# Optimization experiments

Hardware: AMD Instinct MI355X
Metric: run time of the kernel (lower is better)

Reference implementation:

```python
import jax, jax.numpy as jnp
import numpy as np

B, C_IN, C_OUT, STYLE_DIM, H, W = 8, 512, 512, 512, 32, 32

def setup_inputs() -> dict:
    key = jax.random.key(0)
    k = jax.random.split(key, 7)
    x = jax.random.normal(k[0], (B, C_IN, H, W), dtype=jnp.float32)
    style = jax.random.normal(k[1], (B, STYLE_DIM), dtype=jnp.float32)
    noise = jax.random.normal(k[2], (B, 1, 2 * H, 2 * W), dtype=jnp.float32)
    # learned params (Conv2d weight, style_fc Linear, output bias)
    conv_w = jax.random.normal(k[3], (C_OUT, C_IN, 3, 3), dtype=jnp.float32) * 0.05
    fc_w = jax.random.normal(k[4], (C_IN, STYLE_DIM), dtype=jnp.float32) * 0.05
    fc_b = jax.random.normal(k[5], (C_IN,), dtype=jnp.float32) * 0.05
    bias = jnp.zeros((1, C_OUT, 1, 1), dtype=jnp.float32)
    return {"x": x, "style": style, "noise": noise,
            "conv_w": conv_w, "fc_w": fc_w, "fc_b": fc_b, "bias": bias}

def reference(x, style, noise, conv_w, fc_w, fc_b, bias):
    b, c, h, w = x.shape
    o = conv_w.shape[0]
    x = jnp.repeat(jnp.repeat(x, 2, axis=2), 2, axis=3)  # (B, C, 2H, 2W)
    # style modulation: (B, C)
    s = style @ fc_w.T + fc_b
    # per-sample modulated weight (B, O, C, 3, 3)
    wmod = conv_w[None] * (s[:, None, :, None, None] + 1.0)
    # demodulation
    d = jax.lax.rsqrt(jnp.sum(wmod * wmod, axis=(2, 3, 4)) + 1e-8)  # (B, O)
    wmod = wmod * d[:, :, None, None, None]
    # grouped conv: one group per batch sample
    xr = x.reshape(1, b * c, 2 * h, 2 * w)
    wr = wmod.reshape(b * o, c, 3, 3)
    y = jax.lax.conv_general_dilated(
        xr, wr, window_strides=(1, 1), padding='SAME',
        feature_group_count=b,
        dimension_numbers=('NCHW', 'OIHW', 'NCHW'))
    y = y.reshape(b, o, 2 * h, 2 * w) + bias + noise
    return jax.nn.leaky_relu(y, negative_slope=0.2)
```

## Files before the change

kernel.cpp:

```cpp
#include <hip/hip_runtime.h>

typedef short v8s __attribute__((ext_vector_type(8)));
typedef float f32x4 __attribute__((ext_vector_type(4)));
typedef unsigned short ushort_t;

#define BB    8
#define CIN   512
#define COUT  512
#define SDIM  512

#define GLDS(g, l)                                                      \
    __builtin_amdgcn_global_load_lds(                                   \
        (const __attribute__((address_space(1))) void*)(g),             \
        (__attribute__((address_space(3))) void*)(l), 16, 0, 0)

static __device__ __forceinline__ ushort_t f2bf(float f) {
    union { float f; unsigned u; } un; un.f = f;
    unsigned r = un.u + 0x7FFF + ((un.u >> 16) & 1);
    return (ushort_t)(r >> 16);
}

__global__ void k_prep1(const float* __restrict__ style, const float* __restrict__ fc_w,
                        const float* __restrict__ fc_b, float* __restrict__ m,
                        const float* __restrict__ conv_w, float* __restrict__ q,
                        ushort_t* __restrict__ Wb, float* __restrict__ guard) {
    __shared__ float sst[SDIM];
    const int bid = blockIdx.x;
    if (bid < 1024) {
        const int idx = bid * 256 + threadIdx.x;
        const int o = idx >> 9, c = idx & 511;
        float w[3][3];
        const float* wp = conv_w + idx * 9;
        float qs = 0.f;
        for (int i = 0; i < 3; i++)
            for (int j = 0; j < 3; j++) {
                float v = wp[i * 3 + j];
                w[i][j] = v;
                qs += v * v;
            }
        q[idx] = qs;
        const int ch = c >> 5, kg = (c >> 3) & 3, c8 = c & 7;
        for (int py = 0; py < 2; py++) {
            float rs[2][3];
            for (int kx = 0; kx < 3; kx++) {
                rs[0][kx] = (py == 0) ? w[0][kx] : w[0][kx] + w[1][kx];
                rs[1][kx] = (py == 0) ? w[1][kx] + w[2][kx] : w[2][kx];
            }
            for (int px = 0; px < 2; px++) {
                const int p = py * 2 + px;
                float vals[4];
                if (px == 0) {
                    vals[0] = rs[0][0];
                    vals[1] = rs[0][1] + rs[0][2];
                    vals[2] = rs[1][0];
                    vals[3] = rs[1][1] + rs[1][2];
                } else {
                    vals[0] = rs[0][0] + rs[0][1];
                    vals[1] = rs[0][2];
                    vals[2] = rs[1][0] + rs[1][1];
                    vals[3] = rs[1][2];
                }
                for (int t = 0; t < 4; t++)
                    Wb[(size_t)p * (16 * 4 * 4 * 512 * 8) + (size_t)ch * (4 * 4 * 512 * 8)
                       + ((size_t)(t * 4 + kg) * 512 + o) * 8 + c8] = f2bf(vals[t]);
            }
        }
    } else {
        const int sb = bid - 1024;
        const int bx = sb & 1, b = sb >> 1;
        if (sb == 0 && threadIdx.x < 8) guard[threadIdx.x] = 0.f;
        for (int k = threadIdx.x; k < SDIM; k += 256) sst[k] = style[b * SDIM + k];
        __syncthreads();
        const int c = bx * 256 + threadIdx.x;
        float acc = fc_b[c];
        const float* wr = fc_w + c * SDIM;
        for (int k = 0; k < SDIM; k += 4) {
            float4 w4 = *(const float4*)(wr + k);
            acc += w4.x * sst[k] + w4.y * sst[k + 1] + w4.z * sst[k + 2] + w4.w * sst[k + 3];
        }
        m[b * CIN + c] = acc + 1.0f;
    }
}

__global__ void k_prep2(const float* __restrict__ x, const float* __restrict__ m,
                        ushort_t* __restrict__ Xt, const float* __restrict__ q,
                        float* __restrict__ d) {
    __shared__ __align__(16) ushort_t lt[32 * 528];
    const int bid = blockIdx.x, t = threadIdx.x;
    if (bid < 256) {
        const int r = bid & 31, b = bid >> 5;
        for (int s = t; s < 4096; s += 256) {
            const int c = s >> 3, q4 = (s & 7) * 4;
            float4 v = *(const float4*)(x + (((size_t)(b * CIN + c) * 32 + r) * 32 + q4));
            const float mv = m[b * CIN + c];
            lt[(q4 + 0) * 528 + c] = f2bf(v.x * mv);
            lt[(q4 + 1) * 528 + c] = f2bf(v.y * mv);
            lt[(q4 + 2) * 528 + c] = f2bf(v.z * mv);
            lt[(q4 + 3) * 528 + c] = f2bf(v.w * mv);
        }
        __syncthreads();
        for (int s = t; s < 2048; s += 256) {
            const int qq = s >> 6, c8 = s & 63;
            v8s v = *(v8s*)&lt[qq * 528 + c8 * 8];
            *(v8s*)(Xt + (((size_t)(b * 32 + r) * 32 + qq) * 512 + c8 * 8)) = v;
        }
    } else {
        const int w = (bid - 256) * 4 + (t >> 6);
        const int L = t & 63;
        const int b = w >> 9, o = w & 511;
        float4 q1 = *(const float4*)(q + o * 512 + L * 8);
        float4 q2 = *(const float4*)(q + o * 512 + L * 8 + 4);
        float4 m1 = *(const float4*)(m + b * 512 + L * 8);
        float4 m2 = *(const float4*)(m + b * 512 + L * 8 + 4);
        float acc = m1.x * m1.x * q1.x + m1.y * m1.y * q1.y + m1.z * m1.z * q1.z +
                    m1.w * m1.w * q1.w + m2.x * m2.x * q2.x + m2.y * m2.y * q2.y +
                    m2.z * m2.z * q2.z + m2.w * m2.w * q2.w;
        for (int off = 32; off; off >>= 1) acc += __shfl_down(acc, off, 64);
        if (L == 0) d[w] = rsqrtf(acc + 1e-8f);
    }
}

__global__ __launch_bounds__(512, 2) void k_gemm(
    const ushort_t* __restrict__ Xt, const ushort_t* __restrict__ Wb,
    const float* __restrict__ dmod, const float* __restrict__ bias,
    const float* __restrict__ noise, float* __restrict__ out,
    const float* __restrict__ guard) {
    __shared__ __align__(16) ushort_t Wt[4][256 * 32];
    __shared__ __align__(16) ushort_t Xs[4][256 * 32];

    const int tid = threadIdx.x;
    const int L = tid & 63;
    const int wid = tid >> 6;

    const int lin = blockIdx.x + 2 * blockIdx.y + 8 * blockIdx.z;
    const int log = (lin & 7) * 32 + (lin >> 3);
    const int o0 = (log & 1) * 256;
    const int n0 = ((log >> 1) & 3) * 256;
    const int zz = log >> 3;
    const int b = zz >> 2, p = zz & 3;

    const int py = p >> 1, px = p & 1;
    const int ry0 = py ? 0 : -1, cx0 = px ? 0 : -1;
    const int wo = (wid >> 2) * 128, wn = (wid & 3) * 64;
    const int l15 = L & 15, l4 = L >> 4;

    const ushort_t* XtB = Xt + (size_t)b * (32 * 32 * 512);
    const ushort_t* WbP = Wb + (size_t)p * (16 * 4 * 4 * 512 * 8);

    f32x4 acc[8][4];
#pragma unroll
    for (int i = 0; i < 8; i++)
#pragma unroll
        for (int j = 0; j < 4; j++) acc[i][j] = {0.f, 0.f, 0.f, 0.f};

    auto stage1 = [&](int c0, ushort_t* wbuf, ushort_t* xbuf, int i) {
        const int slot = i * 512 + tid;
        const int row = slot >> 2;
        const int tap = (slot & 3) ^ ((row >> 1) & 3);
        const int ldo = (i * 512 + (tid & 448)) * 8;
        const ushort_t* wsrc =
            WbP + (size_t)(c0 >> 5) * (4 * 4 * 512 * 8)
            + ((size_t)((tap * 4 + ((c0 >> 3) & 3)) * 512 + o0 + row)) * 8;
        GLDS(wsrc, wbuf + ldo);
        const int pix = n0 + row;
        const int gr = (pix >> 5) + ry0 + (tap >> 1);
        const int gq = (pix & 31) + cx0 + (tap & 1);
        const ushort_t* xsrc =
            ((unsigned)gr < 32u && (unsigned)gq < 32u)
                ? XtB + (size_t)((gr * 32 + gq) * 512 + c0)
                : (const ushort_t*)guard;
        GLDS(xsrc, xbuf + ldo);
    };

    auto lread = [&](const ushort_t* buf, int row) -> v8s {
        const int gsel = l4 ^ ((row >> 1) & 3);
        return *(const v8s*)&buf[row * 32 + gsel * 8];
    };

#pragma unroll
    for (int pt = 0; pt < 3; ++pt) {
        stage1(pt * 8, Wt[pt], Xs[pt], 0);
        stage1(pt * 8, Wt[pt], Xs[pt], 1);
    }
    asm volatile("s_waitcnt vmcnt(8)" ::: "memory");
    __builtin_amdgcn_s_barrier();

    v8s bfr[4];
    for (int t = 0; t < 64; ++t) {
        const ushort_t* wb = Wt[t & 3];
        const ushort_t* xb = Xs[t & 3];
        ushort_t* wnb = Wt[(t + 3) & 3];
        ushort_t* xnb = Xs[(t + 3) & 3];
        const int c0n = (t + 3) * 8;
        const bool st = (t + 3) < 64;

        {
            v8s af[4];
#pragma unroll
            for (int i = 0; i < 4; i++) af[i] = lread(wb, wo + i * 16 + l15);
#pragma unroll
            for (int j = 0; j < 4; j++) bfr[j] = lread(xb, wn + j * 16 + l15);
            if (st) stage1(c0n, wnb, xnb, 0);
            __builtin_amdgcn_s_barrier();
            asm volatile("s_waitcnt lgkmcnt(0)" ::: "memory");
            __builtin_amdgcn_sched_barrier(0);
            __builtin_amdgcn_s_setprio(1);
#pragma unroll
            for (int i = 0; i < 4; i++)
#pragma unroll
                for (int j = 0; j < 4; j++)
                    acc[i][j] = __builtin_amdgcn_mfma_f32_16x16x32_bf16(
                        af[i], bfr[j], acc[i][j], 0, 0, 0);
            __builtin_amdgcn_s_setprio(0);
            __builtin_amdgcn_s_barrier();
        }
        {
            v8s af[4];
#pragma unroll
            for (int i = 0; i < 4; i++) af[i] = lread(wb, wo + 64 + i * 16 + l15);
            if (st) stage1(c0n, wnb, xnb, 1);
            __builtin_amdgcn_s_barrier();
            asm volatile("s_waitcnt lgkmcnt(0)" ::: "memory");
            __builtin_amdgcn_sched_barrier(0);
            __builtin_amdgcn_s_setprio(1);
#pragma unroll
            for (int i = 0; i < 4; i++)
#pragma unroll
                for (int j = 0; j < 4; j++)
                    acc[4 + i][j] = __builtin_amdgcn_mfma_f32_16x16x32_bf16(
                        af[i], bfr[j], acc[4 + i][j], 0, 0, 0);
            __builtin_amdgcn_s_setprio(0);
            if (t <= 60) asm volatile("s_waitcnt vmcnt(8)" ::: "memory");
            else if (t == 61) asm volatile("s_waitcnt vmcnt(4)" ::: "memory");
            else if (t == 62) asm volatile("s_waitcnt vmcnt(0)" ::: "memory");
            __builtin_amdgcn_s_barrier();
        }
    }

    const float* db = dmod + b * COUT;
    float nz[4];
    int ooff[4];
#pragma unroll
    for (int j = 0; j < 4; j++) {
        const int pix = n0 + wn + j * 16 + l15;
        const int Y = 2 * (pix >> 5) + py, X = 2 * (pix & 31) + px;
        nz[j] = noise[b * 4096 + Y * 64 + X];
        ooff[j] = Y * 64 + X;
    }
    float* outB = out + (size_t)b * COUT * 4096;
#pragma unroll
    for (int i = 0; i < 8; i++) {
        const int ob = o0 + wo + i * 16 + l4 * 4;
        float4 d4 = *(const float4*)(db + ob);
        float4 b4 = *(const float4*)(bias + ob);
        const float dv[4] = {d4.x, d4.y, d4.z, d4.w};
        const float bv[4] = {b4.x, b4.y, b4.z, b4.w};
#pragma unroll
        for (int reg = 0; reg < 4; reg++) {
            float* orow = outB + (size_t)(ob + reg) * 4096;
#pragma unroll
            for (int j = 0; j < 4; j++) {
                float v = acc[i][j][reg] * dv[reg] + bv[reg] + nz[j];
                orow[ooff[j]] = v > 0.f ? v : 0.2f * v;
            }
        }
    }
}

extern "C" void kernel_launch(void* const* d_in, const int* in_sizes, int n_in,
                              void* d_out, int out_size, void* d_ws, size_t ws_size,
                              hipStream_t stream) {
    const float* x      = (const float*)d_in[0];
    const float* style  = (const float*)d_in[1];
    const float* noise  = (const float*)d_in[2];
    const float* conv_w = (const float*)d_in[3];
    const float* fc_w   = (const float*)d_in[4];
    const float* fc_b   = (const float*)d_in[5];
    const float* bias   = (const float*)d_in[6];
    float* out = (float*)d_out;

    float* ws = (float*)d_ws;
    float* m     = ws;
    float* dmod  = ws + 4096;
    float* q     = ws + 8192;
    float* guard = ws + 270336;
    ushort_t* XtU = (ushort_t*)(ws + 270352);
    ushort_t* WbU = XtU + 4194304;

    k_prep1<<<1040, 256, 0, stream>>>(style, fc_w, fc_b, m, conv_w, q, WbU, guard);
    k_prep2<<<1280, 256, 0, stream>>>(x, m, XtU, q, dmod);
    k_gemm<<<dim3(2, 4, 32), 512, 0, stream>>>(XtU, WbU, dmod, bias, noise, out, guard);
}
```

Baseline: 202.0 us.

## Use channel-group-major activation layout and a single-barrier GEMM main loop

The prep kernel now writes activations as [batch][channel-group of 8][pixel][8], so that neighbouring pixels' 16-byte chunks sit next to each other in memory. Before, they were 1 KB apart, which made the gathered global-to-LDS loads in the GEMM strided. The GEMM main loop is also flattened: all LDS fragment reads are issued first, then both staging loads, then all 32 MFMAs, with one barrier per iteration instead of four. The trade-off is that the vmcnt wait is now stricter (vmcnt(4)), which shortens the effective prefetch depth and may expose more memory latency.

```diff
diff --git a/kernel.cpp b/kernel.cpp
--- a/kernel.cpp
+++ b/kernel.cpp
@@ -100,9 +100,9 @@
         }
         __syncthreads();
         for (int s = t; s < 2048; s += 256) {
-            const int qq = s >> 6, c8 = s & 63;
-            v8s v = *(v8s*)&lt[qq * 528 + c8 * 8];
-            *(v8s*)(Xt + (((size_t)(b * 32 + r) * 32 + qq) * 512 + c8 * 8)) = v;
+            const int cg = s >> 5, qq = s & 31;
+            v8s v = *(v8s*)&lt[qq * 528 + cg * 8];
+            *(v8s*)(Xt + (((size_t)(b * 64 + cg) * 1024) + r * 32 + qq) * 8) = v;
         }
     } else {
         const int w = (bid - 256) * 4 + (t >> 6);
@@ -130,7 +130,6 @@
 
     const int tid = threadIdx.x;
     const int L = tid & 63;
-    const int wid = tid >> 6;
 
     const int lin = blockIdx.x + 2 * blockIdx.y + 8 * blockIdx.z;
     const int log = (lin & 7) * 32 + (lin >> 3);
@@ -139,12 +138,13 @@
     const int zz = log >> 3;
     const int b = zz >> 2, p = zz & 3;
 
+    const int wid = tid >> 6;
     const int py = p >> 1, px = p & 1;
     const int ry0 = py ? 0 : -1, cx0 = px ? 0 : -1;
     const int wo = (wid >> 2) * 128, wn = (wid & 3) * 64;
     const int l15 = L & 15, l4 = L >> 4;
 
-    const ushort_t* XtB = Xt + (size_t)b * (32 * 32 * 512);
+    const ushort_t* XtB = Xt + (size_t)b * (64 * 1024 * 8);
     const ushort_t* WbP = Wb + (size_t)p * (16 * 4 * 4 * 512 * 8);
 
     f32x4 acc[8][4];
@@ -167,7 +167,7 @@
         const int gq = (pix & 31) + cx0 + (tap & 1);
         const ushort_t* xsrc =
             ((unsigned)gr < 32u && (unsigned)gq < 32u)
-                ? XtB + (size_t)((gr * 32 + gq) * 512 + c0)
+                ? XtB + ((size_t)(c0 >> 3) * 1024 + gr * 32 + gq) * 8
                 : (const ushort_t*)guard;
         GLDS(xsrc, xbuf + ldo);
     };
@@ -185,56 +185,45 @@
     asm volatile("s_waitcnt vmcnt(8)" ::: "memory");
     __builtin_amdgcn_s_barrier();
 
-    v8s bfr[4];
     for (int t = 0; t < 64; ++t) {
         const ushort_t* wb = Wt[t & 3];
         const ushort_t* xb = Xs[t & 3];
         ushort_t* wnb = Wt[(t + 3) & 3];
         ushort_t* xnb = Xs[(t + 3) & 3];
         const int c0n = (t + 3) * 8;
-        const bool st = (t + 3) < 64;
-
-        {
-            v8s af[4];
-#pragma unroll
-            for (int i = 0; i < 4; i++) af[i] = lread(wb, wo + i * 16 + l15);
-#pragma unroll
-            for (int j = 0; j < 4; j++) bfr[j] = lread(xb, wn + j * 16 + l15);
-            if (st) stage1(c0n, wnb, xnb, 0);
-            __builtin_amdgcn_s_barrier();
-            asm volatile("s_waitcnt lgkmcnt(0)" ::: "memory");
-            __builtin_amdgcn_sched_barrier(0);
-            __builtin_amdgcn_s_setprio(1);
-#pragma unroll
-            for (int i = 0; i < 4; i++)
-#pragma unroll
-                for (int j = 0; j < 4; j++)
-                    acc[i][j] = __builtin_amdgcn_mfma_f32_16x16x32_bf16(
-                        af[i], bfr[j], acc[i][j], 0, 0, 0);
-            __builtin_amdgcn_s_setprio(0);
-            __builtin_amdgcn_s_barrier();
-        }
-        {
-            v8s af[4];
-#pragma unroll
-            for (int i = 0; i < 4; i++) af[i] = lread(wb, wo + 64 + i * 16 + l15);
-            if (st) stage1(c0n, wnb, xnb, 1);
-            __builtin_amdgcn_s_barrier();
-            asm volatile("s_waitcnt lgkmcnt(0)" ::: "memory");
-            __builtin_amdgcn_sched_barrier(0);
-            __builtin_amdgcn_s_setprio(1);
-#pragma unroll
-            for (int i = 0; i < 4; i++)
-#pragma unroll
-                for (int j = 0; j < 4; j++)
-                    acc[4 + i][j] = __builtin_amdgcn_mfma_f32_16x16x32_bf16(
-                        af[i], bfr[j], acc[4 + i][j], 0, 0, 0);
-            __builtin_amdgcn_s_setprio(0);
-            if (t <= 60) asm volatile("s_waitcnt vmcnt(8)" ::: "memory");
-            else if (t == 61) asm volatile("s_waitcnt vmcnt(4)" ::: "memory");
-            else if (t == 62) asm volatile("s_waitcnt vmcnt(0)" ::: "memory");
-            __builtin_amdgcn_s_barrier();
-        }
+
+        v8s af0[4], af1[4], bfr[4];
+#pragma unroll
+        for (int i = 0; i < 4; i++) af0[i] = lread(wb, wo + i * 16 + l15);
+#pragma unroll
+        for (int j = 0; j < 4; j++) bfr[j] = lread(xb, wn + j * 16 + l15);
+#pragma unroll
+        for (int i = 0; i < 4; i++) af1[i] = lread(wb, wo + 64 + i * 16 + l15);
+
+        if (t + 3 < 64) {
+            stage1(c0n, wnb, xnb, 0);
+            stage1(c0n, wnb, xnb, 1);
+        }
+
+        __builtin_amdgcn_s_setprio(1);
+#pragma unroll
+        for (int i = 0; i < 4; i++)
+#pragma unroll
+            for (int j = 0; j < 4; j++)
+                acc[i][j] = __builtin_amdgcn_mfma_f32_16x16x32_bf16(
+                    af0[i], bfr[j], acc[i][j], 0, 0, 0);
+#pragma unroll
+        for (int i = 0; i < 4; i++)
+#pragma unroll
+            for (int j = 0; j < 4; j++)
+                acc[4 + i][j] = __builtin_amdgcn_mfma_f32_16x16x32_bf16(
+                    af1[i], bfr[j], acc[4 + i][j], 0, 0, 0);
+        __builtin_amdgcn_s_setprio(0);
+
+        if (t <= 61) asm volatile("s_waitcnt vmcnt(4)" ::: "memory");
+        else if (t == 62) asm volatile("s_waitcnt vmcnt(0)" ::: "memory");
+
+        __builtin_amdgcn_s_barrier();
     }
 
     const float* db = dmod + b * COUT;
```

Result: faster. 182.2 us (-9.8%).
